# Kernel optimization log

Hardware: AMD Instinct MI355X
Metric: run time of the kernel (lower is better)

## Reference

```python
import jax, jax.numpy as jnp
import numpy as np

H = 256        # hidden_channels
G = 13         # num_input_geofeature
E = 100000     # number of 2nd-order triplets
N = 50000      # num_nodes
DEPTH = 3      # finaldepth
EPS = 1e-5     # BatchNorm eps


def setup_inputs() -> dict:
    key = jax.random.key(0)
    ks = jax.random.split(key, 10)
    d_in = 3 * H + G  # 781
    return {
        "node_feature": jax.random.normal(ks[0], (N, H), jnp.float32),
        "geo_encoding": jax.random.normal(ks[1], (E, G), jnp.float32),
        "edge_index_2rd": jax.random.randint(ks[2], (3, E), 0, N),
        "edx_ij": jax.random.randint(ks[3], (E,), 0, 2 * E),
        "edx_jk": jax.random.randint(ks[4], (E,), 0, 2 * E),
        "att": jax.random.uniform(ks[5], (4,), jnp.float32),
        # 4 branches: layer0 (d_in->H) + DEPTH layers (H->H), xavier-ish init, zero bias
        "W0": jax.random.normal(ks[6], (4, d_in, H), jnp.float32) * (1.0 / np.sqrt(d_in)),
        "b0": jnp.zeros((4, H), jnp.float32),
        "Wh": jax.random.normal(ks[7], (4, DEPTH, H, H), jnp.float32) * (1.0 / np.sqrt(H)),
        "bh": jnp.zeros((4, DEPTH, H), jnp.float32),
        # BatchNorm (eval mode): affine params + running stats, one per layer per branch
        "gamma": jnp.ones((4, DEPTH + 1, H), jnp.float32),
        "beta": jnp.zeros((4, DEPTH + 1, H), jnp.float32),
        "run_mean": jnp.zeros((4, DEPTH + 1, H), jnp.float32),
        "run_var": jnp.ones((4, DEPTH + 1, H), jnp.float32),
        "num_edge_inside": E,
        "num_nodes": N,
    }


def _bn(h, g, b, m, v):
    return (h - m) * jax.lax.rsqrt(v + EPS) * g + b


def reference(node_feature, geo_encoding, edge_index_2rd, edx_ij, edx_jk, att,
              W0, b0, Wh, bh, gamma, beta, run_mean, run_var,
              num_edge_inside, num_nodes):
    i, j, k = edge_index_2rd[0], edge_index_2rd[1], edge_index_2rd[2]
    # gather node triplets + geo features -> [E, 3H+G]
    x = jnp.concatenate(
        [node_feature[i], node_feature[j], node_feature[k], geo_encoding], axis=-1)

    m_ij = edx_ij < num_edge_inside
    m_jk = edx_jk < num_edge_inside
    # 4 mutually-exclusive, exhaustive routing masks: [4, E]
    masks = jnp.stack([m_ij & m_jk, m_ij & ~m_jk, ~m_ij & m_jk, ~m_ij & ~m_jk])

    x_output = jnp.zeros((x.shape[0], H), x.dtype)
    for br in range(4):  # fixed small branch count
        h = jax.nn.relu(_bn(x @ W0[br] + b0[br],
                            gamma[br, 0], beta[br, 0], run_mean[br, 0], run_var[br, 0]))
        for l in range(DEPTH):
            h = jax.nn.relu(_bn(h @ Wh[br, l] + bh[br, l],
                                gamma[br, l + 1], beta[br, l + 1],
                                run_mean[br, l + 1], run_var[br, l + 1]))
        h = jax.nn.leaky_relu(h) * att[br]
        x_output = x_output + jnp.where(masks[br][:, None], h, jnp.zeros((), h.dtype))
    # scatter_add over target node index i -> [num_nodes, H]
    return jax.ops.segment_sum(x_output, i, num_segments=num_nodes)
```

## Files before the change

kernel.cpp:

```cpp
#include <hip/hip_runtime.h>
#include <hip/hip_bf16.h>
#include <stdint.h>

#define HCH 256
#define GEO 13
#define DEPTH 3
#define EPSBN 1e-5f
#define MFMA __builtin_amdgcn_mfma_f32_16x16x32_bf16

typedef __attribute__((ext_vector_type(8))) short short8;
typedef __attribute__((ext_vector_type(4))) float floatx4;

__device__ __forceinline__ short f2bs(float f) {
    unsigned u = __float_as_uint(f);
    unsigned r = (u + 0x7fffu + ((u >> 16) & 1u)) >> 16;
    return (short)r;
}

__global__ void k_zero(float4* out4, int n4, int* cnt) {
    int i = blockIdx.x * blockDim.x + threadIdx.x;
    if (i < n4) out4[i] = make_float4(0.f, 0.f, 0.f, 0.f);
    if (blockIdx.x == 0 && threadIdx.x < 4) cnt[threadIdx.x] = 0;
}

__global__ void k_prep(const float* __restrict__ W0, const float* __restrict__ Wh,
                       const float* __restrict__ b0, const float* __restrict__ bh,
                       const float* __restrict__ gm, const float* __restrict__ bt,
                       const float* __restrict__ mn, const float* __restrict__ vr,
                       const float* __restrict__ att,
                       const float* __restrict__ node, const float* __restrict__ geo,
                       const int* __restrict__ edx_ij, const int* __restrict__ edx_jk,
                       const int* __restrict__ nei_p,
                       short* __restrict__ W0t, short* __restrict__ Wht,
                       float* __restrict__ sc, float* __restrict__ of,
                       short* __restrict__ node_bf, short* __restrict__ geo_bf,
                       int* __restrict__ lists, int* __restrict__ cnt,
                       int E, int d_in_dim, int nb_node, int nb_geo) {
    const int B_W0 = 100, B_WH = 96, B_SC = 16;
    __shared__ short s[32][256];
    int b = blockIdx.x, t = threadIdx.x;
    if (b < B_W0) {
        int c = b % 25, br = b / 25;
        #pragma unroll
        for (int kk = 0; kk < 32; ++kk) {
            int kidx = c * 32 + kk;
            float v = (kidx < d_in_dim) ? W0[((size_t)br * d_in_dim + kidx) * HCH + t] : 0.f;
            s[kk][t] = f2bs(v);
        }
        __syncthreads();
        size_t obase = ((size_t)(b) * 256 + t) * 32;
        #pragma unroll
        for (int g = 0; g < 4; ++g) {
            short8 v;
            #pragma unroll
            for (int j = 0; j < 8; ++j) v[j] = s[g * 8 + j][t];
            *reinterpret_cast<short8*>(W0t + obase + g * 8) = v;
        }
    } else if (b < B_W0 + B_WH) {
        int idx = b - B_W0;
        int c = idx & 7; idx >>= 3;
        int l = idx % 3, br = idx / 3;
        #pragma unroll
        for (int kk = 0; kk < 32; ++kk) {
            float v = Wh[((size_t)(br * DEPTH + l) * HCH + (c * 32 + kk)) * HCH + t];
            s[kk][t] = f2bs(v);
        }
        __syncthreads();
        size_t obase = ((size_t)(b - B_W0) * 256 + t) * 32;
        #pragma unroll
        for (int g = 0; g < 4; ++g) {
            short8 v;
            #pragma unroll
            for (int j = 0; j < 8; ++j) v[j] = s[g * 8 + j][t];
            *reinterpret_cast<short8*>(Wht + obase + g * 8) = v;
        }
    } else if (b < B_W0 + B_WH + B_SC) {
        int idx = (b - B_W0 - B_WH) * 256 + t;
        int col = idx & 255, l = (idx >> 8) & 3, br = idx >> 10;
        int gi = (br * (DEPTH + 1) + l) * HCH + col;
        float sA = gm[gi] * rsqrtf(vr[gi] + EPSBN);
        float bias = (l == 0) ? b0[br * HCH + col] : bh[(br * DEPTH + (l - 1)) * HCH + col];
        float ofv = (bias - mn[gi]) * sA + bt[gi];
        if (l == 3) { float av = att[br]; sA *= av; ofv *= av; }
        sc[idx] = sA;
        of[idx] = ofv;
    } else if (b < B_W0 + B_WH + B_SC + nb_node) {
        size_t i = ((size_t)(b - B_W0 - B_WH - B_SC) * 256 + t) * 8;
        const float4* src = reinterpret_cast<const float4*>(node + i);
        float4 v0 = src[0], v1 = src[1];
        short8 pk;
        pk[0] = f2bs(v0.x); pk[1] = f2bs(v0.y); pk[2] = f2bs(v0.z); pk[3] = f2bs(v0.w);
        pk[4] = f2bs(v1.x); pk[5] = f2bs(v1.y); pk[6] = f2bs(v1.z); pk[7] = f2bs(v1.w);
        *reinterpret_cast<short8*>(node_bf + i) = pk;
    } else if (b < B_W0 + B_WH + B_SC + nb_node + nb_geo) {
        int i = (b - B_W0 - B_WH - B_SC - nb_node) * 256 + t;
        int e = i >> 2, cc = i & 3;
        if (e < E) {
            short8 pk;
            #pragma unroll
            for (int j = 0; j < 8; ++j) {
                int col = cc * 8 + j;
                pk[j] = (col < GEO) ? f2bs(geo[(size_t)e * GEO + col]) : (short)0;
            }
            *reinterpret_cast<short8*>(geo_bf + (size_t)e * 32 + cc * 8) = pk;
        }
    } else {
        int e = (b - (B_W0 + B_WH + B_SC + nb_node + nb_geo)) * 256 + t;
        int NEI = nei_p[0];
        int lane = t & 63;
        int br = -1;
        if (e < E)
            br = ((edx_ij[e] < NEI) ? 0 : 2) + ((edx_jk[e] < NEI) ? 0 : 1);
        unsigned long long lt = (lane == 63) ? 0x7fffffffffffffffull
                                             : ((1ull << lane) - 1ull);
        #pragma unroll
        for (int bb = 0; bb < 4; ++bb) {
            unsigned long long mk = __ballot(br == bb);
            if (mk) {
                int leader = __ffsll((long long)mk) - 1;
                int base = 0;
                if (lane == leader) base = atomicAdd(&cnt[bb], (int)__popcll(mk));
                base = __shfl(base, leader);
                if (br == bb) {
                    int pos = base + (int)__popcll(mk & lt);
                    lists[(size_t)bb * E + pos] = e;
                }
            }
        }
    }
}

__global__ __launch_bounds__(512)
void k_main(const short* __restrict__ node_bf, const short* __restrict__ geo_bf,
            const int* __restrict__ eidx,
            const short* __restrict__ W0t, const short* __restrict__ Wht,
            const float* __restrict__ sc, const float* __restrict__ of,
            const int* __restrict__ lists, const int* __restrict__ cnt,
            float* __restrict__ out, int E) {
    __shared__ __align__(16) short A[64][264];
    __shared__ int s_i[64];
    __shared__ int s_jk[2][64];
    __shared__ int s_e[64];

    int c0 = cnt[0], c1 = cnt[1], c2 = cnt[2], c3 = cnt[3];
    int t0 = (c0 + 63) >> 6, t1 = (c1 + 63) >> 6, t2 = (c2 + 63) >> 6, t3 = (c3 + 63) >> 6;
    int b = blockIdx.x;
    int br, tile, count;
    if (b < t0)                     { br = 0; tile = b;                count = c0; }
    else if (b < t0 + t1)           { br = 1; tile = b - t0;           count = c1; }
    else if (b < t0 + t1 + t2)      { br = 2; tile = b - t0 - t1;      count = c2; }
    else if (b < t0 + t1 + t2 + t3) { br = 3; tile = b - t0 - t1 - t2; count = c3; }
    else return;
    int m = count - tile * 64; if (m > 64) m = 64;

    int t = threadIdx.x;
    if (t < 64) {
        int e = (t < m) ? lists[(size_t)br * E + (size_t)tile * 64 + t] : 0;
        s_e[t] = (t < m) ? e : -1;
        s_i[t] = eidx[e];
        s_jk[0][t] = eidx[E + e];
        s_jk[1][t] = eidx[2 * E + e];
    }
    __syncthreads();

    int wv = t >> 6, lane = t & 63, quad = lane >> 4, l16 = lane & 15;
    int rbase = t >> 5, cc8 = (t & 31) * 8;

    floatx4 acc[4][2];
    #pragma unroll
    for (int rt = 0; rt < 4; ++rt)
        #pragma unroll
        for (int ct = 0; ct < 2; ++ct)
            #pragma unroll
            for (int r = 0; r < 4; ++r) acc[rt][ct][r] = 0.f;

    int boff[2];
    #pragma unroll
    for (int ct = 0; ct < 2; ++ct)
        boff[ct] = (wv * 32 + ct * 16 + l16) * 32 + quad * 8;

    auto do_chunks8 = [&](const short* Wbase) {
        short8 bb[3][2];
        #pragma unroll
        for (int ct = 0; ct < 2; ++ct) {
            bb[0][ct] = *reinterpret_cast<const short8*>(Wbase + boff[ct]);
            bb[1][ct] = *reinterpret_cast<const short8*>(Wbase + 8192 + boff[ct]);
        }
        #pragma unroll
        for (int c = 0; c < 8; ++c) {
            if (c + 2 < 8) {
                const short* Bn = Wbase + (size_t)(c + 2) * 8192;
                #pragma unroll
                for (int ct = 0; ct < 2; ++ct)
                    bb[(c + 2) % 3][ct] = *reinterpret_cast<const short8*>(Bn + boff[ct]);
            }
            short8 af[4];
            #pragma unroll
            for (int rt = 0; rt < 4; ++rt)
                af[rt] = *reinterpret_cast<const short8*>(&A[rt * 16 + l16][c * 32 + quad * 8]);
            #pragma unroll
            for (int rt = 0; rt < 4; ++rt)
                #pragma unroll
                for (int ct = 0; ct < 2; ++ct)
                    acc[rt][ct] = MFMA(af[rt], bb[c % 3][ct], acc[rt][ct], 0, 0, 0);
        }
    };
    auto do_chunk1 = [&](const short* Wbase) {
        short8 bc[2];
        #pragma unroll
        for (int ct = 0; ct < 2; ++ct)
            bc[ct] = *reinterpret_cast<const short8*>(Wbase + boff[ct]);
        short8 af[4];
        #pragma unroll
        for (int rt = 0; rt < 4; ++rt)
            af[rt] = *reinterpret_cast<const short8*>(&A[rt * 16 + l16][quad * 8]);
        #pragma unroll
        for (int rt = 0; rt < 4; ++rt)
            #pragma unroll
            for (int ct = 0; ct < 2; ++ct)
                acc[rt][ct] = MFMA(af[rt], bc[ct], acc[rt][ct], 0, 0, 0);
    };

    short8 g[2][4];
    short8 ggeo;
    {
        #pragma unroll
        for (int it = 0; it < 4; ++it)
            g[0][it] = *reinterpret_cast<const short8*>(
                node_bf + (size_t)s_i[it * 16 + rbase] * HCH + cc8);
    }
    int grow = t >> 2, gcc = t & 3;
    for (int p = 0; p < 4; ++p) {
        __syncthreads();
        if (p < 3) {
            #pragma unroll
            for (int it = 0; it < 4; ++it)
                *reinterpret_cast<short8*>(&A[it * 16 + rbase][cc8]) = g[p & 1][it];
        } else if (t < 256) {
            *reinterpret_cast<short8*>(&A[grow][gcc * 8]) = ggeo;
        }
        __syncthreads();
        if (p < 2) {
            const int* idxs = s_jk[p];
            #pragma unroll
            for (int it = 0; it < 4; ++it)
                g[(p + 1) & 1][it] = *reinterpret_cast<const short8*>(
                    node_bf + (size_t)idxs[it * 16 + rbase] * HCH + cc8);
        } else if (p == 2 && t < 256) {
            int e = s_e[grow];
            if (e >= 0)
                ggeo = *reinterpret_cast<const short8*>(geo_bf + (size_t)e * 32 + gcc * 8);
            else {
                #pragma unroll
                for (int j = 0; j < 8; ++j) ggeo[j] = 0;
            }
        }
        if (p < 3) do_chunks8(W0t + (size_t)(br * 25 + p * 8) * 8192);
        else       do_chunk1(W0t + (size_t)(br * 25 + 24) * 8192);
    }

    for (int l = 0; l < 4; ++l) {
        float sv[2], ov[2];
        #pragma unroll
        for (int ct = 0; ct < 2; ++ct) {
            int col = wv * 32 + ct * 16 + l16;
            sv[ct] = sc[(br * 4 + l) * HCH + col];
            ov[ct] = of[(br * 4 + l) * HCH + col];
        }
        if (l < 3) {
            __syncthreads();
            #pragma unroll
            for (int rt = 0; rt < 4; ++rt)
                #pragma unroll
                for (int ct = 0; ct < 2; ++ct) {
                    int col = wv * 32 + ct * 16 + l16;
                    #pragma unroll
                    for (int r = 0; r < 4; ++r) {
                        float h = fmaxf(acc[rt][ct][r] * sv[ct] + ov[ct], 0.f);
                        A[rt * 16 + quad * 4 + r][col] = f2bs(h);
                        acc[rt][ct][r] = 0.f;
                    }
                }
            __syncthreads();
            do_chunks8(Wht + (size_t)((br * 3 + l) * 8) * 8192);
        } else {
            #pragma unroll
            for (int rt = 0; rt < 4; ++rt)
                #pragma unroll
                for (int r = 0; r < 4; ++r) {
                    int row = rt * 16 + quad * 4 + r;
                    if (row < m) {
                        float* orow = out + (size_t)s_i[row] * HCH + wv * 32 + l16;
                        #pragma unroll
                        for (int ct = 0; ct < 2; ++ct) {
                            float h = fmaxf(acc[rt][ct][r] * sv[ct] + ov[ct], 0.f);
                            atomicAdd(orow + ct * 16, h);
                        }
                    }
                }
        }
    }
}

extern "C" void kernel_launch(void* const* d_in, const int* in_sizes, int n_in,
                              void* d_out, int out_size, void* d_ws, size_t ws_size,
                              hipStream_t stream) {
    const float* node  = (const float*)d_in[0];
    const float* geo   = (const float*)d_in[1];
    const int*   eidx  = (const int*)d_in[2];
    const int*   edxij = (const int*)d_in[3];
    const int*   edxjk = (const int*)d_in[4];
    const float* att   = (const float*)d_in[5];
    const float* W0    = (const float*)d_in[6];
    const float* b0    = (const float*)d_in[7];
    const float* Wh    = (const float*)d_in[8];
    const float* bh    = (const float*)d_in[9];
    const float* gm    = (const float*)d_in[10];
    const float* bt    = (const float*)d_in[11];
    const float* mn    = (const float*)d_in[12];
    const float* vr    = (const float*)d_in[13];
    const int*   neip  = (const int*)d_in[14];

    int E = in_sizes[3];
    int N = in_sizes[0] / HCH;
    int d_in_dim = in_sizes[6] / (4 * HCH);

    uint8_t* w = (uint8_t*)d_ws;
    size_t off = 0;
    short* W0t  = (short*)(w + off); off += (size_t)4 * 25 * 256 * 32 * 2;
    short* Wht  = (short*)(w + off); off += (size_t)4 * 3 * 8 * 256 * 32 * 2;
    float* sc   = (float*)(w + off); off += 4096 * 4;
    float* of   = (float*)(w + off); off += 4096 * 4;
    int*   lists= (int*)(w + off);   off += (size_t)4 * E * 4;
    int*   cnt  = (int*)(w + off);   off += 16;
    short* node_bf = (short*)(w + off); off += (size_t)N * HCH * 2;
    short* geo_bf  = (short*)(w + off); off += (size_t)E * 32 * 2;

    float* out = (float*)d_out;
    int n4 = out_size / 4;
    k_zero<<<(n4 + 255) / 256, 256, 0, stream>>>((float4*)out, n4, cnt);

    int nb_node = N / 8;
    int nb_geo  = (4 * E + 255) / 256;
    int nb_cmp  = (E + 255) / 256;
    k_prep<<<100 + 96 + 16 + nb_node + nb_geo + nb_cmp, 256, 0, stream>>>(
        W0, Wh, b0, bh, gm, bt, mn, vr, att, node, geo, edxij, edxjk, neip,
        W0t, Wht, sc, of, node_bf, geo_bf, lists, cnt, E, d_in_dim, nb_node, nb_geo);

    int T = (E >> 6) + 8;
    k_main<<<T, 512, 0, stream>>>(node_bf, geo_bf, eidx, W0t, Wht,
                                  sc, of, lists, cnt, out, E);
}
```

Baseline: 384.5 us.

## Halve workgroup to 4 waves with 64-column warp tiles in main GEMM kernel

The main fused MLP kernel now runs 256 threads (4 waves) per 64-row tile instead of 8, and each wave computes a 64-column slab (4x4 MFMA tiles) instead of 32 columns. Each A-fragment LDS read now feeds twice as many MFMAs, and the weight prefetch is reduced from a 3-deep to a 2-deep (double) buffer. Gather loads are redistributed so each thread issues 8 row-chunk loads. The cost is higher VGPR pressure from 64 accumulator floats per lane, fewer waves per block to hide gather and weight-load latency, and more atomics per thread in the epilogue.

```diff
diff --git a/kernel.cpp b/kernel.cpp
--- a/kernel.cpp
+++ b/kernel.cpp
@@ -130,7 +130,7 @@
     }
 }
 
-__global__ __launch_bounds__(512)
+__global__ __launch_bounds__(256)
 void k_main(const short* __restrict__ node_bf, const short* __restrict__ geo_bf,
             const int* __restrict__ eidx,
             const short* __restrict__ W0t, const short* __restrict__ Wht,
@@ -164,35 +164,32 @@
     __syncthreads();
 
     int wv = t >> 6, lane = t & 63, quad = lane >> 4, l16 = lane & 15;
-    int rbase = t >> 5, cc8 = (t & 31) * 8;
-
-    floatx4 acc[4][2];
+
+    floatx4 acc[4][4];
     #pragma unroll
     for (int rt = 0; rt < 4; ++rt)
         #pragma unroll
-        for (int ct = 0; ct < 2; ++ct)
+        for (int ct = 0; ct < 4; ++ct)
             #pragma unroll
             for (int r = 0; r < 4; ++r) acc[rt][ct][r] = 0.f;
 
-    int boff[2];
+    int boff[4];
     #pragma unroll
-    for (int ct = 0; ct < 2; ++ct)
-        boff[ct] = (wv * 32 + ct * 16 + l16) * 32 + quad * 8;
+    for (int ct = 0; ct < 4; ++ct)
+        boff[ct] = (wv * 64 + ct * 16 + l16) * 32 + quad * 8;
 
     auto do_chunks8 = [&](const short* Wbase) {
-        short8 bb[3][2];
-        #pragma unroll
-        for (int ct = 0; ct < 2; ++ct) {
-            bb[0][ct] = *reinterpret_cast<const short8*>(Wbase + boff[ct]);
-            bb[1][ct] = *reinterpret_cast<const short8*>(Wbase + 8192 + boff[ct]);
-        }
+        short8 bcur[4], bnxt[4];
+        #pragma unroll
+        for (int ct = 0; ct < 4; ++ct)
+            bcur[ct] = *reinterpret_cast<const short8*>(Wbase + boff[ct]);
         #pragma unroll
         for (int c = 0; c < 8; ++c) {
-            if (c + 2 < 8) {
-                const short* Bn = Wbase + (size_t)(c + 2) * 8192;
-                #pragma unroll
-                for (int ct = 0; ct < 2; ++ct)
-                    bb[(c + 2) % 3][ct] = *reinterpret_cast<const short8*>(Bn + boff[ct]);
+            if (c + 1 < 8) {
+                const short* Bn = Wbase + (size_t)(c + 1) * 8192;
+                #pragma unroll
+                for (int ct = 0; ct < 4; ++ct)
+                    bnxt[ct] = *reinterpret_cast<const short8*>(Bn + boff[ct]);
             }
             short8 af[4];
             #pragma unroll
@@ -201,14 +198,18 @@
             #pragma unroll
             for (int rt = 0; rt < 4; ++rt)
                 #pragma unroll
-                for (int ct = 0; ct < 2; ++ct)
-                    acc[rt][ct] = MFMA(af[rt], bb[c % 3][ct], acc[rt][ct], 0, 0, 0);
+                for (int ct = 0; ct < 4; ++ct)
+                    acc[rt][ct] = MFMA(af[rt], bcur[ct], acc[rt][ct], 0, 0, 0);
+            if (c + 1 < 8) {
+                #pragma unroll
+                for (int ct = 0; ct < 4; ++ct) bcur[ct] = bnxt[ct];
+            }
         }
     };
     auto do_chunk1 = [&](const short* Wbase) {
-        short8 bc[2];
-        #pragma unroll
-        for (int ct = 0; ct < 2; ++ct)
+        short8 bc[4];
+        #pragma unroll
+        for (int ct = 0; ct < 4; ++ct)
             bc[ct] = *reinterpret_cast<const short8*>(Wbase + boff[ct]);
         short8 af[4];
         #pragma unroll
@@ -217,36 +218,40 @@
         #pragma unroll
         for (int rt = 0; rt < 4; ++rt)
             #pragma unroll
-            for (int ct = 0; ct < 2; ++ct)
+            for (int ct = 0; ct < 4; ++ct)
                 acc[rt][ct] = MFMA(af[rt], bc[ct], acc[rt][ct], 0, 0, 0);
     };
 
-    short8 g[2][4];
+    short8 g[8];
     short8 ggeo;
-    {
-        #pragma unroll
-        for (int it = 0; it < 4; ++it)
-            g[0][it] = *reinterpret_cast<const short8*>(
-                node_bf + (size_t)s_i[it * 16 + rbase] * HCH + cc8);
+    #pragma unroll
+    for (int it = 0; it < 8; ++it) {
+        int job = it * 256 + t, row = job >> 5, cc = job & 31;
+        g[it] = *reinterpret_cast<const short8*>(
+            node_bf + (size_t)s_i[row] * HCH + cc * 8);
     }
     int grow = t >> 2, gcc = t & 3;
     for (int p = 0; p < 4; ++p) {
         __syncthreads();
         if (p < 3) {
             #pragma unroll
-            for (int it = 0; it < 4; ++it)
-                *reinterpret_cast<short8*>(&A[it * 16 + rbase][cc8]) = g[p & 1][it];
-        } else if (t < 256) {
+            for (int it = 0; it < 8; ++it) {
+                int job = it * 256 + t, row = job >> 5, cc = job & 31;
+                *reinterpret_cast<short8*>(&A[row][cc * 8]) = g[it];
+            }
+        } else {
             *reinterpret_cast<short8*>(&A[grow][gcc * 8]) = ggeo;
         }
         __syncthreads();
         if (p < 2) {
             const int* idxs = s_jk[p];
             #pragma unroll
-            for (int it = 0; it < 4; ++it)
-                g[(p + 1) & 1][it] = *reinterpret_cast<const short8*>(
-                    node_bf + (size_t)idxs[it * 16 + rbase] * HCH + cc8);
-        } else if (p == 2 && t < 256) {
+            for (int it = 0; it < 8; ++it) {
+                int job = it * 256 + t, row = job >> 5, cc = job & 31;
+                g[it] = *reinterpret_cast<const short8*>(
+                    node_bf + (size_t)idxs[row] * HCH + cc * 8);
+            }
+        } else if (p == 2) {
             int e = s_e[grow];
             if (e >= 0)
                 ggeo = *reinterpret_cast<const short8*>(geo_bf + (size_t)e * 32 + gcc * 8);
@@ -260,10 +265,10 @@
     }
 
     for (int l = 0; l < 4; ++l) {
-        float sv[2], ov[2];
-        #pragma unroll
-        for (int ct = 0; ct < 2; ++ct) {
-            int col = wv * 32 + ct * 16 + l16;
+        float sv[4], ov[4];
+        #pragma unroll
+        for (int ct = 0; ct < 4; ++ct) {
+            int col = wv * 64 + ct * 16 + l16;
             sv[ct] = sc[(br * 4 + l) * HCH + col];
             ov[ct] = of[(br * 4 + l) * HCH + col];
         }
@@ -272,8 +277,8 @@
             #pragma unroll
             for (int rt = 0; rt < 4; ++rt)
                 #pragma unroll
-                for (int ct = 0; ct < 2; ++ct) {
-                    int col = wv * 32 + ct * 16 + l16;
+                for (int ct = 0; ct < 4; ++ct) {
+                    int col = wv * 64 + ct * 16 + l16;
                     #pragma unroll
                     for (int r = 0; r < 4; ++r) {
                         float h = fmaxf(acc[rt][ct][r] * sv[ct] + ov[ct], 0.f);
@@ -290,9 +295,9 @@
                 for (int r = 0; r < 4; ++r) {
                     int row = rt * 16 + quad * 4 + r;
                     if (row < m) {
-                        float* orow = out + (size_t)s_i[row] * HCH + wv * 32 + l16;
+                        float* orow = out + (size_t)s_i[row] * HCH + wv * 64 + l16;
                         #pragma unroll
-                        for (int ct = 0; ct < 2; ++ct) {
+                        for (int ct = 0; ct < 4; ++ct) {
                             float h = fmaxf(acc[rt][ct][r] * sv[ct] + ov[ct], 0.f);
                             atomicAdd(orow + ct * 16, h);
                         }
@@ -348,6 +353,6 @@
         W0t, Wht, sc, of, node_bf, geo_bf, lists, cnt, E, d_in_dim, nb_node, nb_geo);
 
     int T = (E >> 6) + 8;
-    k_main<<<T, 512, 0, stream>>>(node_bf, geo_bf, eidx, W0t, Wht,
+    k_main<<<T, 256, 0, stream>>>(node_bf, geo_bf, eidx, W0t, Wht,
                                   sc, of, lists, cnt, out, E);
 }
```

Measured after the change: 463.8 us. +20.6%, slower.
